# Kernel tuning notes

Hardware: AMD Instinct MI355X
Metric: run time of the kernel (lower is better)

## Reference

```python
import jax, jax.numpy as jnp
import numpy as np

NUM_HEADS = 8
EPS = 1e-12  # matches torch F.normalize eps


def setup_inputs() -> dict:
    key = jax.random.key(0)
    ks = jax.random.split(key, 4)
    B, C, H, W = 32, 384, 32, 32
    x = jax.random.normal(ks[0], (B, C, H, W), dtype=jnp.float32)
    w_qkv = jax.random.normal(ks[1], (3 * C, C), dtype=jnp.float32) * (1.0 / np.sqrt(C))
    b_qkv = jnp.zeros((3 * C,), dtype=jnp.float32)
    temperature = jnp.ones((NUM_HEADS, 1, 1), dtype=jnp.float32)
    w_proj = jax.random.normal(ks[2], (C, C), dtype=jnp.float32) * (1.0 / np.sqrt(C))
    b_proj = jnp.zeros((C,), dtype=jnp.float32)
    return {"x": x, "w_qkv": w_qkv, "b_qkv": b_qkv, "temperature": temperature,
            "w_proj": w_proj, "b_proj": b_proj}


def _l2norm_tokens(t):
    # L2-normalize over the token axis N (last dim), torch F.normalize semantics
    n = jnp.sqrt(jnp.sum(t * t, axis=-1, keepdims=True))
    return t / jnp.maximum(n, EPS)


def reference(x, w_qkv, b_qkv, temperature, w_proj, b_proj):
    B, C, H, W = x.shape
    N = H * W
    nh = NUM_HEADS
    dh = C // nh
    xf = x.reshape(B, C, N)
    # 1x1 conv == channel GEMM: [B,3C,N]
    qkv = jnp.einsum('oc,bcn->bon', w_qkv, xf) + b_qkv[:, None]
    qkv = qkv.reshape(B, 3, nh, dh, N)
    q, k, v = qkv[:, 0], qkv[:, 1], qkv[:, 2]  # each [B,nh,dh,N]
    q = _l2norm_tokens(q)
    k = _l2norm_tokens(k)
    # cross-covariance: contract over N -> small [B,nh,dh,dh]
    attn = jnp.einsum('bhdn,bhen->bhde', q, k) * temperature
    attn = jax.nn.softmax(attn, axis=-1)
    out = jnp.einsum('bhde,bhen->bhdn', attn, v).reshape(B, C, N)
    out = jnp.einsum('oc,bcn->bon', w_proj, out) + b_proj[:, None]
    return x + out.reshape(B, C, H, W)
```

## Files before the change

### kernel.cpp

```cpp
#include <hip/hip_runtime.h>
#include <hip/hip_bf16.h>
#include <stdint.h>

#define BATCH  32
#define CDIM   384
#define NTOK   1024
#define NHEADS 8
#define DH     48

using f32x4  = __attribute__((ext_vector_type(4))) float;
using bf16x8 = __attribute__((ext_vector_type(8))) short;
using u16x4  = __attribute__((ext_vector_type(4))) uint16_t;
using u16x8  = __attribute__((ext_vector_type(8))) uint16_t;

__device__ __forceinline__ uint16_t f2bf(float f) {
  __hip_bfloat16 h = __float2bfloat16(f);
  return *reinterpret_cast<uint16_t*>(&h);
}
__device__ __forceinline__ float bf2f(uint16_t u) {
  return __uint_as_float(((uint32_t)u) << 16);
}

#define GLL16(gsrc, ldst)                                                    \
  __builtin_amdgcn_global_load_lds(                                          \
      (const __attribute__((address_space(1))) void*)(gsrc),                 \
      (__attribute__((address_space(3))) void*)(ldst), 16, 0, 0)

__global__ __launch_bounds__(256) void k_transpose_x(const float* __restrict__ x,
                                                     uint16_t* __restrict__ xT,
                                                     uint16_t* __restrict__ xbf,
                                                     int use_xbf,
                                                     const float* __restrict__ wqkv,
                                                     const float* __restrict__ wproj,
                                                     uint16_t* __restrict__ wq,
                                                     uint16_t* __restrict__ wp) {
  int tid = threadIdx.x;
  if (blockIdx.y == 6) {
    int id = blockIdx.x + 16 * blockIdx.z;
    int n1 = 3 * CDIM * CDIM, n2 = CDIM * CDIM;
    for (int i = id * 256 + tid; i < n1 + n2; i += 512 * 256) {
      if (i < n1) wq[i] = f2bf(wqkv[i]);
      else        wp[i - n1] = f2bf(wproj[i - n1]);
    }
    return;
  }
  __shared__ float t[64][65];
  int n0 = blockIdx.x * 64;
  int c0 = blockIdx.y * 64;
  int b  = blockIdx.z;
  const float* xb = x + (size_t)b * CDIM * NTOK;
  uint16_t* xbb = xbf + (size_t)b * CDIM * NTOK;
#pragma unroll
  for (int p = 0; p < 4; ++p) {
    int r  = (tid >> 4) + p * 16;
    int cc = (tid & 15) * 4;
    float4 v = *(const float4*)(xb + (size_t)(c0 + r) * NTOK + n0 + cc);
    t[r][cc + 0] = v.x; t[r][cc + 1] = v.y; t[r][cc + 2] = v.z; t[r][cc + 3] = v.w;
    if (use_xbf) {
      u16x4 o; o[0] = f2bf(v.x); o[1] = f2bf(v.y); o[2] = f2bf(v.z); o[3] = f2bf(v.w);
      *(u16x4*)(xbb + (size_t)(c0 + r) * NTOK + n0 + cc) = o;
    }
  }
  __syncthreads();
  uint16_t* xTb = xT + (size_t)b * NTOK * CDIM;
#pragma unroll
  for (int p = 0; p < 2; ++p) {
    int n  = (tid >> 3) + p * 32;
    int cb = (tid & 7) * 8;
    u16x8 o;
#pragma unroll
    for (int j = 0; j < 8; ++j) o[j] = f2bf(t[cb + j][n]);
    *(u16x8*)(xTb + (size_t)(n0 + n) * CDIM + c0 + cb) = o;
  }
}

__device__ __forceinline__ void qkv_stage(const uint16_t* __restrict__ A,
                                          const uint16_t* __restrict__ B,
                                          uint16_t* buf, int kt, int tid) {
  uint16_t* lA = buf;
  uint16_t* lB = buf + 8192;
#pragma unroll
  for (int i = 0; i < 2; ++i) {
    int ch = tid + 512 * i;
    int r  = ch >> 3;
    int cs = (((ch & 7) ^ (r & 7)) << 3);
    GLL16(A + (size_t)r * 384 + kt + cs, lA + (size_t)ch * 8);
  }
#pragma unroll
  for (int i = 0; i < 2; ++i) {
    int ch = tid + 512 * i;
    int r  = ch >> 3;
    int cs = (((ch & 7) ^ (r & 7)) << 3);
    GLL16(B + (size_t)r * 384 + kt + cs, lB + (size_t)ch * 8);
  }
}

__global__ __launch_bounds__(512) void k_qkv(const uint16_t* __restrict__ Wq,
                                             const uint16_t* __restrict__ xT,
                                             const float* __restrict__ bqkv,
                                             uint16_t* __restrict__ qk,
                                             uint16_t* __restrict__ vT) {
  __shared__ uint16_t lds[2][16384];
  int tid = threadIdx.x;
  int id  = blockIdx.x;
  int xcd = id & 7, idx = id >> 3;
  int jt  = xcd * 32 + (idx & 31);
  int bm  = idx >> 5;
  int o0 = bm * 128, j0 = jt * 128;
  const uint16_t* A = Wq + (size_t)o0 * 384;
  const uint16_t* B = xT + (size_t)j0 * 384;

  int w = tid >> 6, lane = tid & 63;
  int wr = w >> 2, wc = w & 3;
  int lr = lane & 15, g = lane >> 4;

  f32x4 acc[4][2];
#pragma unroll
  for (int i = 0; i < 4; ++i)
#pragma unroll
    for (int j = 0; j < 2; ++j) acc[i][j] = (f32x4){0.f, 0.f, 0.f, 0.f};

  qkv_stage(A, B, lds[0], 0, tid);
  asm volatile("s_waitcnt vmcnt(0)" ::: "memory");
  __builtin_amdgcn_s_barrier();
#pragma unroll
  for (int t = 0; t < 6; ++t) {
    if (t < 5) qkv_stage(A, B, lds[(t + 1) & 1], (t + 1) * 64, tid);
    const uint16_t* lA = &lds[t & 1][0];
    const uint16_t* lB = &lds[t & 1][8192];
#pragma unroll
    for (int ks = 0; ks < 2; ++ks) {
      bf16x8 af[4], bfr[2];
#pragma unroll
      for (int mt = 0; mt < 4; ++mt) {
        int row = wr * 64 + mt * 16 + lr;
        int sl  = (((ks * 4 + g) ^ (row & 7)) << 3);
        af[mt] = *(const bf16x8*)(lA + (size_t)row * 64 + sl);
      }
#pragma unroll
      for (int nt = 0; nt < 2; ++nt) {
        int row = wc * 32 + nt * 16 + lr;
        int sl  = (((ks * 4 + g) ^ (row & 7)) << 3);
        bfr[nt] = *(const bf16x8*)(lB + (size_t)row * 64 + sl);
      }
#pragma unroll
      for (int mt = 0; mt < 4; ++mt)
#pragma unroll
        for (int nt = 0; nt < 2; ++nt)
          acc[mt][nt] = __builtin_amdgcn_mfma_f32_16x16x32_bf16(af[mt], bfr[nt], acc[mt][nt], 0, 0, 0);
    }
    asm volatile("s_waitcnt vmcnt(0)" ::: "memory");
    __builtin_amdgcn_s_barrier();
  }

#pragma unroll
  for (int mt = 0; mt < 4; ++mt) {
    int ob = o0 + wr * 64 + mt * 16 + g * 4;
    float b0 = bqkv[ob + 0], b1 = bqkv[ob + 1], b2 = bqkv[ob + 2], b3 = bqkv[ob + 3];
#pragma unroll
    for (int nt = 0; nt < 2; ++nt) {
      int j = j0 + wc * 32 + nt * 16 + lr;
      int b = j >> 10, n = j & 1023;
      f32x4 v = acc[mt][nt];
      float v0 = v[0] + b0, v1 = v[1] + b1, v2 = v[2] + b2, v3 = v[3] + b3;
      if (ob < 768) {
        uint16_t* dst = qk + ((size_t)(b * 768 + ob) * 1024 + n);
        dst[0] = f2bf(v0); dst[1024] = f2bf(v1); dst[2048] = f2bf(v2); dst[3072] = f2bf(v3);
      } else {
        int oc = ob - 768;
        int h = oc / 48, d = oc % 48;
        u16x4 p;
        p[0] = f2bf(v0); p[1] = f2bf(v1); p[2] = f2bf(v2); p[3] = f2bf(v3);
        *(u16x4*)(vT + ((size_t)((b * 8 + h) * 1024 + n) * 48 + d)) = p;
      }
    }
  }
}

__device__ __forceinline__ void gemm_tile_128(const uint16_t* __restrict__ A,
                                              const uint16_t* __restrict__ B,
                                              uint16_t* ldsA, uint16_t* ldsB,
                                              f32x4 acc[4][4], int tid) {
  const int K = 384;
  int w = tid >> 6, lane = tid & 63;
  int wr = w >> 1, wc = w & 1;
  int lr = lane & 15, g = lane >> 4;
  for (int kt = 0; kt < K; kt += 64) {
    __syncthreads();
#pragma unroll
    for (int iss = 0; iss < 4; ++iss) {
      int ch = tid + 256 * iss;
      int r  = ch >> 3;
      int cs = (((ch & 7) ^ (r & 7)) << 3);
      GLL16(A + (size_t)r * K + kt + cs, ldsA + (size_t)ch * 8);
      GLL16(B + (size_t)r * K + kt + cs, ldsB + (size_t)ch * 8);
    }
    __syncthreads();
#pragma unroll
    for (int ks = 0; ks < 2; ++ks) {
      bf16x8 af[4], bfr[4];
#pragma unroll
      for (int mt = 0; mt < 4; ++mt) {
        int row = wr * 64 + mt * 16 + lr;
        int sl  = (((ks * 4 + g) ^ (row & 7)) << 3);
        af[mt] = *(const bf16x8*)(ldsA + (size_t)row * 64 + sl);
      }
#pragma unroll
      for (int nt = 0; nt < 4; ++nt) {
        int row = wc * 64 + nt * 16 + lr;
        int sl  = (((ks * 4 + g) ^ (row & 7)) << 3);
        bfr[nt] = *(const bf16x8*)(ldsB + (size_t)row * 64 + sl);
      }
#pragma unroll
      for (int mt = 0; mt < 4; ++mt)
#pragma unroll
        for (int nt = 0; nt < 4; ++nt)
          acc[mt][nt] = __builtin_amdgcn_mfma_f32_16x16x32_bf16(af[mt], bfr[nt], acc[mt][nt], 0, 0, 0);
    }
  }
}

__global__ __launch_bounds__(512) void k_attn(const uint16_t* __restrict__ qk,
                                              const uint16_t* __restrict__ vT,
                                              const float* __restrict__ temperature,
                                              uint16_t* __restrict__ aT) {
  __shared__ float Sp[8][48][49];
  __shared__ float Sf[48][49];
  __shared__ uint16_t P[48][72];
  __shared__ float nrm[96];
  int tid = threadIdx.x, w = tid >> 6, lane = tid & 63;
  int bh = blockIdx.x, b = bh >> 3, h = bh & 7;
  const uint16_t* qbase = qk + (size_t)(b * 768 + h * 48) * 1024;
  const uint16_t* kbase = qbase + (size_t)384 * 1024;

  for (int r = w; r < 96; r += 8) {
    const uint16_t* row = (r < 48) ? (qbase + (size_t)r * 1024)
                                   : (kbase + (size_t)(r - 48) * 1024);
    float s = 0.f;
#pragma unroll
    for (int jj = 0; jj < 4; ++jj) {
      u16x4 u = *(const u16x4*)(row + (size_t)(jj * 64 + lane) * 4);
#pragma unroll
      for (int e = 0; e < 4; ++e) { float f = bf2f(u[e]); s += f * f; }
    }
#pragma unroll
    for (int off = 32; off > 0; off >>= 1) s += __shfl_down(s, off);
    if (lane == 0) nrm[r] = fmaxf(sqrtf(s), 1e-12f);
  }

  int lr = lane & 15, g = lane >> 4;
  int nbase = w * 128;
  f32x4 sacc[3][3];
#pragma unroll
  for (int i = 0; i < 3; ++i)
#pragma unroll
    for (int j = 0; j < 3; ++j) sacc[i][j] = (f32x4){0.f, 0.f, 0.f, 0.f};
#pragma unroll
  for (int ks = 0; ks < 4; ++ks) {
    bf16x8 aq[3], bk[3];
#pragma unroll
    for (int mt = 0; mt < 3; ++mt)
      aq[mt] = *(const bf16x8*)(qbase + (size_t)(mt * 16 + lr) * 1024 + nbase + ks * 32 + g * 8);
#pragma unroll
    for (int et = 0; et < 3; ++et)
      bk[et] = *(const bf16x8*)(kbase + (size_t)(et * 16 + lr) * 1024 + nbase + ks * 32 + g * 8);
#pragma unroll
    for (int mt = 0; mt < 3; ++mt)
#pragma unroll
      for (int et = 0; et < 3; ++et)
        sacc[mt][et] = __builtin_amdgcn_mfma_f32_16x16x32_bf16(aq[mt], bk[et], sacc[mt][et], 0, 0, 0);
  }
#pragma unroll
  for (int mt = 0; mt < 3; ++mt)
#pragma unroll
    for (int et = 0; et < 3; ++et)
#pragma unroll
      for (int r = 0; r < 4; ++r)
        Sp[w][mt * 16 + g * 4 + r][et * 16 + lr] = sacc[mt][et][r];
  __syncthreads();

  float temp = temperature[h];
  for (int idx = tid; idx < 48 * 48; idx += 512) {
    int d = idx / 48, e = idx - d * 48;
    float s = 0.f;
#pragma unroll
    for (int ww = 0; ww < 8; ++ww) s += Sp[ww][d][e];
    Sf[d][e] = s * temp / (nrm[d] * nrm[48 + e]);
  }
  __syncthreads();

  if (tid < 48) {
    int d = tid;
    float m = -1e30f;
    for (int e = 0; e < 48; ++e) m = fmaxf(m, Sf[d][e]);
    float sum = 0.f;
    for (int e = 0; e < 48; ++e) { float v = __expf(Sf[d][e] - m); sum += v; Sf[d][e] = v; }
    float inv = 1.f / sum;
    for (int e = 0; e < 48; ++e) P[d][e] = f2bf(Sf[d][e] * inv);
    for (int e = 48; e < 64; ++e) P[d][e] = 0;
  }
  __syncthreads();

  bf16x8 af[3][2];
#pragma unroll
  for (int mt = 0; mt < 3; ++mt)
#pragma unroll
    for (int ks = 0; ks < 2; ++ks)
      af[mt][ks] = *(const bf16x8*)(&P[mt * 16 + lr][ks * 32 + g * 8]);
  const uint16_t* vb = vT + (size_t)(b * 8 + h) * 1024 * 48;
  bf16x8 zf;
#pragma unroll
  for (int i = 0; i < 8; ++i) zf[i] = 0;
#pragma unroll
  for (int nt = 0; nt < 8; ++nt) {
    int n = w * 128 + nt * 16 + lr;
    bf16x8 bv[2];
    bv[0] = *(const bf16x8*)(vb + (size_t)n * 48 + g * 8);
    int eb1 = 32 + g * 8;
    bv[1] = (eb1 < 48) ? *(const bf16x8*)(vb + (size_t)n * 48 + eb1) : zf;
    f32x4 o[3];
#pragma unroll
    for (int mt = 0; mt < 3; ++mt) o[mt] = (f32x4){0.f, 0.f, 0.f, 0.f};
#pragma unroll
    for (int ks = 0; ks < 2; ++ks)
#pragma unroll
      for (int mt = 0; mt < 3; ++mt)
        o[mt] = __builtin_amdgcn_mfma_f32_16x16x32_bf16(af[mt][ks], bv[ks], o[mt], 0, 0, 0);
#pragma unroll
    for (int mt = 0; mt < 3; ++mt) {
      int c = h * 48 + mt * 16 + g * 4;
      u16x4 p;
#pragma unroll
      for (int r = 0; r < 4; ++r) p[r] = f2bf(o[mt][r]);
      *(u16x4*)(aT + ((size_t)(b * 1024 + n) * 384 + c)) = p;
    }
  }
}

__global__ __launch_bounds__(256) void k_proj(const uint16_t* __restrict__ Wp,
                                              const uint16_t* __restrict__ aT,
                                              const float* __restrict__ bproj,
                                              const uint16_t* __restrict__ xbf,
                                              const float* __restrict__ x,
                                              float* __restrict__ out,
                                              int use_xbf) {
  __shared__ uint16_t ldsA[128 * 64];
  __shared__ uint16_t ldsB[128 * 64];
  int tid = threadIdx.x;
  int id  = blockIdx.x;
  int xcd = id & 7, idx = id >> 3;
  int jt  = xcd * 32 + (idx & 31);
  int bm  = idx >> 5;
  int o0 = bm * 128, j0 = jt * 128;
  f32x4 acc[4][4];
#pragma unroll
  for (int i = 0; i < 4; ++i)
#pragma unroll
    for (int j = 0; j < 4; ++j) acc[i][j] = (f32x4){0.f, 0.f, 0.f, 0.f};

  gemm_tile_128(Wp + (size_t)o0 * 384, aT + (size_t)j0 * 384, ldsA, ldsB, acc, tid);

  int w = tid >> 6, lane = tid & 63;
  int wr = w >> 1, wc = w & 1, lr = lane & 15, g = lane >> 4;
#pragma unroll
  for (int mt = 0; mt < 4; ++mt) {
    int ob = o0 + wr * 64 + mt * 16 + g * 4;
    float b0 = bproj[ob + 0], b1 = bproj[ob + 1], b2 = bproj[ob + 2], b3 = bproj[ob + 3];
#pragma unroll
    for (int nt = 0; nt < 4; ++nt) {
      int j = j0 + wc * 64 + nt * 16 + lr;
      int b = j >> 10, n = j & 1023;
      f32x4 v = acc[mt][nt];
      size_t i0 = (size_t)(b * 384 + ob) * 1024 + n;
      float r0, r1, r2, r3;
      if (use_xbf) {
        r0 = bf2f(xbf[i0]); r1 = bf2f(xbf[i0 + 1024]);
        r2 = bf2f(xbf[i0 + 2048]); r3 = bf2f(xbf[i0 + 3072]);
      } else {
        r0 = x[i0]; r1 = x[i0 + 1024]; r2 = x[i0 + 2048]; r3 = x[i0 + 3072];
      }
      __builtin_nontemporal_store(v[0] + b0 + r0, &out[i0]);
      __builtin_nontemporal_store(v[1] + b1 + r1, &out[i0 + 1024]);
      __builtin_nontemporal_store(v[2] + b2 + r2, &out[i0 + 2048]);
      __builtin_nontemporal_store(v[3] + b3 + r3, &out[i0 + 3072]);
    }
  }
}

extern "C" void kernel_launch(void* const* d_in, const int* in_sizes, int n_in,
                              void* d_out, int out_size, void* d_ws, size_t ws_size,
                              hipStream_t stream) {
  const float* x     = (const float*)d_in[0];
  const float* wqkv  = (const float*)d_in[1];
  const float* bqkv  = (const float*)d_in[2];
  const float* temp  = (const float*)d_in[3];
  const float* wproj = (const float*)d_in[4];
  const float* bproj = (const float*)d_in[5];
  float* out = (float*)d_out;

  char* ws = (char*)d_ws;
  size_t off = 0;
  auto alloc = [&](size_t bytes) -> char* {
    char* p = ws + off;
    off += (bytes + 255) & ~(size_t)255;
    return p;
  };
  uint16_t* xT    = (uint16_t*)alloc((size_t)BATCH * NTOK * CDIM * 2);
  uint16_t* wq_bf = (uint16_t*)alloc((size_t)3 * CDIM * CDIM * 2);
  uint16_t* wp_bf = (uint16_t*)alloc((size_t)CDIM * CDIM * 2);
  uint16_t* qkbuf = (uint16_t*)alloc((size_t)BATCH * 768 * NTOK * 2);
  uint16_t* vTbuf = (uint16_t*)alloc((size_t)BATCH * NHEADS * NTOK * DH * 2);
  size_t xbf_bytes = (size_t)BATCH * CDIM * NTOK * 2;
  int use_xbf = (off + xbf_bytes <= ws_size) ? 1 : 0;
  uint16_t* xbf = use_xbf ? (uint16_t*)alloc(xbf_bytes) : (uint16_t*)xT;
  uint16_t* aT  = xT;

  k_transpose_x<<<dim3(NTOK / 64, 7, BATCH), dim3(256), 0, stream>>>(
      x, xT, xbf, use_xbf, wqkv, wproj, wq_bf, wp_bf);
  k_qkv<<<dim3(2304), dim3(512), 0, stream>>>(wq_bf, xT, bqkv, qkbuf, vTbuf);
  k_attn<<<dim3(256), dim3(512), 0, stream>>>(qkbuf, vTbuf, temp, aT);
  k_proj<<<dim3(768), dim3(256), 0, stream>>>(wp_bf, aT, bproj, xbf, x, out, use_xbf);
}
```

Before: 129.0 us.

## Fuse x transpose/bf16 conversion into QKV GEMM, keep token tile resident in LDS

Removes the separate transpose kernel that wrote a bf16 transposed copy of x to global memory. Each QKV block now loads a 128-token slab of fp32 x straight into LDS, converts it to a swizzled bf16 B tile that stays resident, and loops over all nine 128-row weight blocks while double-buffering only the weight tiles. Weight conversion moves to its own small kernel. This cuts global traffic for xT, but the grid shrinks to 256 large blocks using about 130KB of LDS each, which lowers occupancy and makes the blocks serialize over the weight loop.

```diff
diff --git a/kernel.cpp b/kernel.cpp
--- a/kernel.cpp
+++ b/kernel.cpp
@@ -26,152 +26,158 @@
       (const __attribute__((address_space(1))) void*)(gsrc),                 \
       (__attribute__((address_space(3))) void*)(ldst), 16, 0, 0)
 
-__global__ __launch_bounds__(256) void k_transpose_x(const float* __restrict__ x,
-                                                     uint16_t* __restrict__ xT,
-                                                     uint16_t* __restrict__ xbf,
-                                                     int use_xbf,
-                                                     const float* __restrict__ wqkv,
-                                                     const float* __restrict__ wproj,
-                                                     uint16_t* __restrict__ wq,
-                                                     uint16_t* __restrict__ wp) {
+__global__ __launch_bounds__(256) void k_convert_w(const float* __restrict__ wqkv,
+                                                   const float* __restrict__ wproj,
+                                                   uint16_t* __restrict__ wq,
+                                                   uint16_t* __restrict__ wp) {
+  int n1 = 3 * CDIM * CDIM;
+  int n2 = CDIM * CDIM;
+  int stride = gridDim.x * 256;
+  for (int i = blockIdx.x * 256 + threadIdx.x; i < n1 + n2; i += stride) {
+    if (i < n1) wq[i] = f2bf(wqkv[i]);
+    else        wp[i - n1] = f2bf(wproj[i - n1]);
+  }
+}
+
+__global__ __launch_bounds__(512) void k_qkv_fused(const float* __restrict__ x,
+                                                   const uint16_t* __restrict__ Wq,
+                                                   const float* __restrict__ bqkv,
+                                                   uint16_t* __restrict__ qk,
+                                                   uint16_t* __restrict__ vT,
+                                                   uint16_t* __restrict__ xbf,
+                                                   int use_xbf) {
+  __shared__ uint8_t smem[133120];
+  uint16_t* lB  = (uint16_t*)smem;
+  float*    xf  = (float*)(smem + 100352);
+  uint16_t* lA0 = (uint16_t*)(smem + 100352);
+  uint16_t* lA1 = (uint16_t*)(smem + 100352 + 16384);
+
   int tid = threadIdx.x;
-  if (blockIdx.y == 6) {
-    int id = blockIdx.x + 16 * blockIdx.z;
-    int n1 = 3 * CDIM * CDIM, n2 = CDIM * CDIM;
-    for (int i = id * 256 + tid; i < n1 + n2; i += 512 * 256) {
-      if (i < n1) wq[i] = f2bf(wqkv[i]);
-      else        wp[i - n1] = f2bf(wproj[i - n1]);
-    }
-    return;
-  }
-  __shared__ float t[64][65];
-  int n0 = blockIdx.x * 64;
-  int c0 = blockIdx.y * 64;
-  int b  = blockIdx.z;
-  const float* xb = x + (size_t)b * CDIM * NTOK;
-  uint16_t* xbb = xbf + (size_t)b * CDIM * NTOK;
-#pragma unroll
-  for (int p = 0; p < 4; ++p) {
-    int r  = (tid >> 4) + p * 16;
-    int cc = (tid & 15) * 4;
-    float4 v = *(const float4*)(xb + (size_t)(c0 + r) * NTOK + n0 + cc);
-    t[r][cc + 0] = v.x; t[r][cc + 1] = v.y; t[r][cc + 2] = v.z; t[r][cc + 3] = v.w;
+  int jt  = blockIdx.x;
+  int b = jt >> 3, n0 = (jt & 7) * 128;
+  const float* xsrc = x + (size_t)b * CDIM * NTOK + n0;
+
+  for (int ck = 0; ck < 6; ++ck) {
+    int c0 = ck * 64;
+#pragma unroll
+    for (int i = 0; i < 4; ++i) {
+      int ch = tid + 512 * i;
+      int r  = ch >> 5;
+      int cc = (ch & 31) * 4;
+      GLL16(xsrc + (size_t)(c0 + r) * NTOK + cc, (uint16_t*)xf + (size_t)ch * 8);
+    }
+    asm volatile("s_waitcnt vmcnt(0)" ::: "memory");
+    __syncthreads();
+    {
+      int n = tid & 127, coct = tid >> 7;
+      float v[16];
+#pragma unroll
+      for (int j = 0; j < 16; ++j) v[j] = xf[(size_t)(coct * 16 + j) * 128 + n];
+#pragma unroll
+      for (int g2 = 0; g2 < 2; ++g2) {
+        u16x8 pk;
+#pragma unroll
+        for (int j = 0; j < 8; ++j) pk[j] = f2bf(v[g2 * 8 + j]);
+        int s   = coct * 2 + g2;
+        int off = c0 + ((s ^ (n & 7)) << 3);
+        *(u16x8*)(lB + (size_t)n * 392 + off) = pk;
+      }
+    }
     if (use_xbf) {
-      u16x4 o; o[0] = f2bf(v.x); o[1] = f2bf(v.y); o[2] = f2bf(v.z); o[3] = f2bf(v.w);
-      *(u16x4*)(xbb + (size_t)(c0 + r) * NTOK + n0 + cc) = o;
-    }
-  }
-  __syncthreads();
-  uint16_t* xTb = xT + (size_t)b * NTOK * CDIM;
-#pragma unroll
-  for (int p = 0; p < 2; ++p) {
-    int n  = (tid >> 3) + p * 32;
-    int cb = (tid & 7) * 8;
-    u16x8 o;
-#pragma unroll
-    for (int j = 0; j < 8; ++j) o[j] = f2bf(t[cb + j][n]);
-    *(u16x8*)(xTb + (size_t)(n0 + n) * CDIM + c0 + cb) = o;
-  }
-}
-
-__device__ __forceinline__ void qkv_stage(const uint16_t* __restrict__ A,
-                                          const uint16_t* __restrict__ B,
-                                          uint16_t* buf, int kt, int tid) {
-  uint16_t* lA = buf;
-  uint16_t* lB = buf + 8192;
-#pragma unroll
-  for (int i = 0; i < 2; ++i) {
-    int ch = tid + 512 * i;
-    int r  = ch >> 3;
-    int cs = (((ch & 7) ^ (r & 7)) << 3);
-    GLL16(A + (size_t)r * 384 + kt + cs, lA + (size_t)ch * 8);
-  }
-#pragma unroll
-  for (int i = 0; i < 2; ++i) {
-    int ch = tid + 512 * i;
-    int r  = ch >> 3;
-    int cs = (((ch & 7) ^ (r & 7)) << 3);
-    GLL16(B + (size_t)r * 384 + kt + cs, lB + (size_t)ch * 8);
-  }
-}
-
-__global__ __launch_bounds__(512) void k_qkv(const uint16_t* __restrict__ Wq,
-                                             const uint16_t* __restrict__ xT,
-                                             const float* __restrict__ bqkv,
-                                             uint16_t* __restrict__ qk,
-                                             uint16_t* __restrict__ vT) {
-  __shared__ uint16_t lds[2][16384];
-  int tid = threadIdx.x;
-  int id  = blockIdx.x;
-  int xcd = id & 7, idx = id >> 3;
-  int jt  = xcd * 32 + (idx & 31);
-  int bm  = idx >> 5;
-  int o0 = bm * 128, j0 = jt * 128;
-  const uint16_t* A = Wq + (size_t)o0 * 384;
-  const uint16_t* B = xT + (size_t)j0 * 384;
+      int cr = tid >> 3;
+      int nc = (tid & 7) * 16;
+      uint16_t* dst = xbf + (size_t)b * CDIM * NTOK + (size_t)(c0 + cr) * NTOK + n0 + nc;
+#pragma unroll
+      for (int q = 0; q < 2; ++q) {
+        u16x8 pk;
+#pragma unroll
+        for (int j = 0; j < 8; ++j) pk[j] = f2bf(xf[(size_t)cr * 128 + nc + q * 8 + j]);
+        *(u16x8*)(dst + q * 8) = pk;
+      }
+    }
+    __syncthreads();
+  }
 
   int w = tid >> 6, lane = tid & 63;
-  int wr = w >> 2, wc = w & 3;
+  int wr = w >> 1, wc = w & 1;
   int lr = lane & 15, g = lane >> 4;
 
-  f32x4 acc[4][2];
-#pragma unroll
-  for (int i = 0; i < 4; ++i)
-#pragma unroll
-    for (int j = 0; j < 2; ++j) acc[i][j] = (f32x4){0.f, 0.f, 0.f, 0.f};
-
-  qkv_stage(A, B, lds[0], 0, tid);
-  asm volatile("s_waitcnt vmcnt(0)" ::: "memory");
-  __builtin_amdgcn_s_barrier();
-#pragma unroll
-  for (int t = 0; t < 6; ++t) {
-    if (t < 5) qkv_stage(A, B, lds[(t + 1) & 1], (t + 1) * 64, tid);
-    const uint16_t* lA = &lds[t & 1][0];
-    const uint16_t* lB = &lds[t & 1][8192];
-#pragma unroll
-    for (int ks = 0; ks < 2; ++ks) {
-      bf16x8 af[4], bfr[2];
-#pragma unroll
-      for (int mt = 0; mt < 4; ++mt) {
-        int row = wr * 64 + mt * 16 + lr;
-        int sl  = (((ks * 4 + g) ^ (row & 7)) << 3);
-        af[mt] = *(const bf16x8*)(lA + (size_t)row * 64 + sl);
-      }
-#pragma unroll
-      for (int nt = 0; nt < 2; ++nt) {
-        int row = wc * 32 + nt * 16 + lr;
-        int sl  = (((ks * 4 + g) ^ (row & 7)) << 3);
-        bfr[nt] = *(const bf16x8*)(lB + (size_t)row * 64 + sl);
-      }
-#pragma unroll
-      for (int mt = 0; mt < 4; ++mt)
-#pragma unroll
-        for (int nt = 0; nt < 2; ++nt)
-          acc[mt][nt] = __builtin_amdgcn_mfma_f32_16x16x32_bf16(af[mt], bfr[nt], acc[mt][nt], 0, 0, 0);
+  for (int bm = 0; bm < 9; ++bm) {
+    const uint16_t* A = Wq + (size_t)bm * 128 * 384;
+    f32x4 acc[2][4];
+#pragma unroll
+    for (int i = 0; i < 2; ++i)
+#pragma unroll
+      for (int j = 0; j < 4; ++j) acc[i][j] = (f32x4){0.f, 0.f, 0.f, 0.f};
+
+#pragma unroll
+    for (int i = 0; i < 2; ++i) {
+      int ch = tid + 512 * i;
+      int r  = ch >> 3;
+      int cs = (((ch & 7) ^ (r & 7)) << 3);
+      GLL16(A + (size_t)r * 384 + cs, lA0 + (size_t)ch * 8);
     }
     asm volatile("s_waitcnt vmcnt(0)" ::: "memory");
     __builtin_amdgcn_s_barrier();
-  }
-
-#pragma unroll
-  for (int mt = 0; mt < 4; ++mt) {
-    int ob = o0 + wr * 64 + mt * 16 + g * 4;
-    float b0 = bqkv[ob + 0], b1 = bqkv[ob + 1], b2 = bqkv[ob + 2], b3 = bqkv[ob + 3];
-#pragma unroll
-    for (int nt = 0; nt < 2; ++nt) {
-      int j = j0 + wc * 32 + nt * 16 + lr;
-      int b = j >> 10, n = j & 1023;
-      f32x4 v = acc[mt][nt];
-      float v0 = v[0] + b0, v1 = v[1] + b1, v2 = v[2] + b2, v3 = v[3] + b3;
-      if (ob < 768) {
-        uint16_t* dst = qk + ((size_t)(b * 768 + ob) * 1024 + n);
-        dst[0] = f2bf(v0); dst[1024] = f2bf(v1); dst[2048] = f2bf(v2); dst[3072] = f2bf(v3);
-      } else {
-        int oc = ob - 768;
-        int h = oc / 48, d = oc % 48;
-        u16x4 p;
-        p[0] = f2bf(v0); p[1] = f2bf(v1); p[2] = f2bf(v2); p[3] = f2bf(v3);
-        *(u16x4*)(vT + ((size_t)((b * 8 + h) * 1024 + n) * 48 + d)) = p;
+#pragma unroll
+    for (int t = 0; t < 6; ++t) {
+      uint16_t* cur = (t & 1) ? lA1 : lA0;
+      uint16_t* nxt = (t & 1) ? lA0 : lA1;
+      if (t < 5) {
+#pragma unroll
+        for (int i = 0; i < 2; ++i) {
+          int ch = tid + 512 * i;
+          int r  = ch >> 3;
+          int cs = (((ch & 7) ^ (r & 7)) << 3);
+          GLL16(A + (size_t)r * 384 + (t + 1) * 64 + cs, nxt + (size_t)ch * 8);
+        }
+      }
+      int kt = t * 64;
+#pragma unroll
+      for (int ks = 0; ks < 2; ++ks) {
+        bf16x8 af[2], bfr[4];
+#pragma unroll
+        for (int mt = 0; mt < 2; ++mt) {
+          int row = wr * 32 + mt * 16 + lr;
+          int sl  = (((ks * 4 + g) ^ (row & 7)) << 3);
+          af[mt] = *(const bf16x8*)(cur + (size_t)row * 64 + sl);
+        }
+#pragma unroll
+        for (int nt = 0; nt < 4; ++nt) {
+          int row = wc * 64 + nt * 16 + lr;
+          int off = kt + (((ks * 4 + g) ^ (row & 7)) << 3);
+          bfr[nt] = *(const bf16x8*)(lB + (size_t)row * 392 + off);
+        }
+#pragma unroll
+        for (int mt = 0; mt < 2; ++mt)
+#pragma unroll
+          for (int nt = 0; nt < 4; ++nt)
+            acc[mt][nt] = __builtin_amdgcn_mfma_f32_16x16x32_bf16(af[mt], bfr[nt], acc[mt][nt], 0, 0, 0);
+      }
+      asm volatile("s_waitcnt vmcnt(0)" ::: "memory");
+      __builtin_amdgcn_s_barrier();
+    }
+
+    int o0 = bm * 128;
+#pragma unroll
+    for (int mt = 0; mt < 2; ++mt) {
+      int ob = o0 + wr * 32 + mt * 16 + g * 4;
+      float b0 = bqkv[ob + 0], b1 = bqkv[ob + 1], b2 = bqkv[ob + 2], b3 = bqkv[ob + 3];
+#pragma unroll
+      for (int nt = 0; nt < 4; ++nt) {
+        int n = n0 + wc * 64 + nt * 16 + lr;
+        f32x4 v = acc[mt][nt];
+        float v0 = v[0] + b0, v1 = v[1] + b1, v2 = v[2] + b2, v3 = v[3] + b3;
+        if (ob < 768) {
+          uint16_t* dst = qk + ((size_t)(b * 768 + ob) * 1024 + n);
+          dst[0] = f2bf(v0); dst[1024] = f2bf(v1); dst[2048] = f2bf(v2); dst[3072] = f2bf(v3);
+        } else {
+          int oc = ob - 768;
+          int h = oc / 48, d = oc % 48;
+          u16x4 p;
+          p[0] = f2bf(v0); p[1] = f2bf(v1); p[2] = f2bf(v2); p[3] = f2bf(v3);
+          *(u16x4*)(vT + ((size_t)((b * 8 + h) * 1024 + n) * 48 + d)) = p;
+        }
       }
     }
   }
@@ -405,19 +411,17 @@
     off += (bytes + 255) & ~(size_t)255;
     return p;
   };
-  uint16_t* xT    = (uint16_t*)alloc((size_t)BATCH * NTOK * CDIM * 2);
   uint16_t* wq_bf = (uint16_t*)alloc((size_t)3 * CDIM * CDIM * 2);
   uint16_t* wp_bf = (uint16_t*)alloc((size_t)CDIM * CDIM * 2);
   uint16_t* qkbuf = (uint16_t*)alloc((size_t)BATCH * 768 * NTOK * 2);
   uint16_t* vTbuf = (uint16_t*)alloc((size_t)BATCH * NHEADS * NTOK * DH * 2);
+  uint16_t* aT    = (uint16_t*)alloc((size_t)BATCH * NTOK * CDIM * 2);
   size_t xbf_bytes = (size_t)BATCH * CDIM * NTOK * 2;
   int use_xbf = (off + xbf_bytes <= ws_size) ? 1 : 0;
-  uint16_t* xbf = use_xbf ? (uint16_t*)alloc(xbf_bytes) : (uint16_t*)xT;
-  uint16_t* aT  = xT;
-
-  k_transpose_x<<<dim3(NTOK / 64, 7, BATCH), dim3(256), 0, stream>>>(
-      x, xT, xbf, use_xbf, wqkv, wproj, wq_bf, wp_bf);
-  k_qkv<<<dim3(2304), dim3(512), 0, stream>>>(wq_bf, xT, bqkv, qkbuf, vTbuf);
+  uint16_t* xbf = use_xbf ? (uint16_t*)alloc(xbf_bytes) : (uint16_t*)aT;
+
+  k_convert_w<<<dim3(576), dim3(256), 0, stream>>>(wqkv, wproj, wq_bf, wp_bf);
+  k_qkv_fused<<<dim3(256), dim3(512), 0, stream>>>(x, wq_bf, bqkv, qkbuf, vTbuf, xbf, use_xbf);
   k_attn<<<dim3(256), dim3(512), 0, stream>>>(qkbuf, vTbuf, temp, aT);
   k_proj<<<dim3(768), dim3(256), 0, stream>>>(wp_bf, aT, bproj, xbf, x, out, use_xbf);
 }
```

Result: slower. 137.4 us (+6.5%).
